# Kernel optimization log

Measured on AMD Instinct MI355X. Metric: run time of the kernel, lower is better.

Reference implementation:

```python
import jax, jax.numpy as jnp
import numpy as np

V, L_MAX, D_MODEL, N_LAYER, N_STATE, EXPAND = 49408, 512, 768, 4, 16, 2
D_INNER = EXPAND * D_MODEL            # 1536
DT_RANK = -(-D_MODEL // 16)           # 48 ('auto' = ceil(d_model/16))
D_CONV = 4
B, T = 4, 256
EPS = 1e-5


def setup_inputs() -> dict:
    key = jax.random.key(0)
    ks = jax.random.split(key, 10)
    s = 0.02
    inp = {
        "input_ids": jax.random.randint(ks[0], (B, T), 0, V),
        "emb": jax.random.normal(ks[1], (V, D_MODEL), jnp.float32) * s,
        "pos_emb": jax.random.normal(ks[2], (1, L_MAX, D_MODEL), jnp.float32) * s,
        "in_proj_w": jax.random.normal(ks[3], (N_LAYER, 2 * D_INNER, D_MODEL), jnp.float32) * s,
        "conv_w": jax.random.normal(ks[4], (N_LAYER, D_INNER, D_CONV), jnp.float32) * s,
        "conv_b": jnp.zeros((N_LAYER, D_INNER), jnp.float32),
        "x_proj_w": jax.random.normal(ks[5], (N_LAYER, DT_RANK + 2 * N_STATE, D_INNER), jnp.float32) * s,
        "dt_proj_w": jax.random.normal(ks[6], (N_LAYER, D_INNER, DT_RANK), jnp.float32) * s,
        "dt_proj_b": jnp.full((N_LAYER, D_INNER), -4.6, jnp.float32),  # softplus(-4.6)~0.01, inside [dt_min,dt_max]
        # S4D-real init: A_log[l,d,n] = log(n+1)
        "A_log": jnp.tile(jnp.log(jnp.arange(1, N_STATE + 1, dtype=jnp.float32)), (N_LAYER, D_INNER, 1)),
        "D_skip": jnp.ones((N_LAYER, D_INNER), jnp.float32),
        "out_proj_w": jax.random.normal(ks[7], (N_LAYER, D_MODEL, D_INNER), jnp.float32) * s,
        "norm_w": jnp.ones((D_MODEL,), jnp.float32),
    }
    return inp


def _causal_dwconv(x, w, b):
    # x: (B, C, T), w: (C, K) depthwise, b: (C,) ; causal pad K-1 on the left
    out = jax.lax.conv_general_dilated(
        x, w[:, None, :], window_strides=(1,), padding=[(D_CONV - 1, 0)],
        feature_group_count=x.shape[1], dimension_numbers=("NCH", "OIH", "NCH"))
    return out + b[None, :, None]


def _selective_scan(deltaA, dBx, Cm):
    # deltaA, dBx: (B, T, D, N); Cm: (B, T, N) -> y: (B, T, D)
    def step(h, t_in):
        dA, dbx, c = t_in
        h = dA * h + dbx                          # (B, D, N)
        y = jnp.einsum("bdn,bn->bd", h, c)
        return h, y
    h0 = jnp.zeros(deltaA.shape[:1] + deltaA.shape[2:], deltaA.dtype)
    _, ys = jax.lax.scan(step, h0, (deltaA.swapaxes(0, 1), dBx.swapaxes(0, 1), Cm.swapaxes(0, 1)))
    return ys.swapaxes(0, 1)


def _mamba_block(x, ipw, cw, cb, xpw, dpw, dpb, A_log, Dp, opw):
    # x: (B, T, d_model)
    xz = jnp.einsum("btd,ed->bte", x, ipw)        # (B, T, 2*D_INNER)
    xi, z = jnp.split(xz, 2, axis=-1)
    xi = jax.nn.silu(_causal_dwconv(xi.swapaxes(1, 2), cw, cb)).swapaxes(1, 2)  # (B, T, D_INNER)
    x_dbl = jnp.einsum("btd,ed->bte", xi, xpw)    # (B, T, DT_RANK + 2N)
    dt, Bm, Cm = jnp.split(x_dbl, [DT_RANK, DT_RANK + N_STATE], axis=-1)
    dt = jax.nn.softplus(jnp.einsum("btr,dr->btd", dt, dpw) + dpb)              # (B, T, D_INNER)
    A = -jnp.exp(A_log)                            # (D_INNER, N)
    deltaA = jnp.exp(dt[..., None] * A)            # (B, T, D_INNER, N)
    dBx = dt[..., None] * Bm[:, :, None, :] * xi[..., None]                     # (B, T, D_INNER, N)
    y = _selective_scan(deltaA, dBx, Cm) + Dp * xi
    y = y * jax.nn.silu(z)
    return jnp.einsum("btd,ed->bte", y, opw)       # (B, T, d_model)


def reference(input_ids, emb, pos_emb, in_proj_w, conv_w, conv_b, x_proj_w,
              dt_proj_w, dt_proj_b, A_log, D_skip, out_proj_w, norm_w):
    Tlen = input_ids.shape[1]
    x = emb[input_ids] + pos_emb[:, :Tlen, :]
    for l in range(N_LAYER):
        x = x + _mamba_block(x, in_proj_w[l], conv_w[l], conv_b[l], x_proj_w[l],
                             dt_proj_w[l], dt_proj_b[l], A_log[l], D_skip[l], out_proj_w[l])
    # RMSNormGated with no gate -> plain RMSNorm
    x = x * jax.lax.rsqrt(jnp.mean(x * x, axis=-1, keepdims=True) + EPS) * norm_w
    return x
```

## Files before the change

### kernel.cpp

```cpp
#include <hip/hip_runtime.h>
#include <math.h>

#define TLEN 256
#define BATCH 4
#define DMODEL 768
#define DINNER 1536
#define NSTATE 16
#define DTRANK 48
#define NLAYER 4
#define NTOK 1024

#define S_IP 2359296
#define S_OP 1179648
#define S_XP2 196608
#define WL (S_IP + S_OP + S_XP2)
#define NB_W (WL / 1024)
#define NB_WALL (NB_W * NLAYER)
#define NB_E (NTOK * DMODEL / 256)

typedef __bf16 bf16x8 __attribute__((ext_vector_type(8)));
typedef float f32x4 __attribute__((ext_vector_type(4)));

__device__ inline unsigned short f2b(float f) {
    union { float f; unsigned u; } v;
    v.f = f;
    unsigned r = (v.u + 0x7fffu + ((v.u >> 16) & 1u)) >> 16;
    return (unsigned short)r;
}
__device__ inline float b2f(unsigned short u) {
    union { unsigned u; float f; } v;
    v.u = ((unsigned)u) << 16;
    return v.f;
}

__device__ inline void gload16(const void* g, void* l) {
    __builtin_amdgcn_global_load_lds(
        (const __attribute__((address_space(1))) void*)g,
        (__attribute__((address_space(3))) void*)l, 16, 0, 0);
}

__device__ inline float red16(float p) {
    p += __int_as_float(__builtin_amdgcn_update_dpp(0, __float_as_int(p), 0xB1, 0xf, 0xf, true));
    p += __int_as_float(__builtin_amdgcn_update_dpp(0, __float_as_int(p), 0x4E, 0xf, 0xf, true));
    p += __int_as_float(__builtin_amdgcn_update_dpp(0, __float_as_int(p), 0x124, 0xf, 0xf, true));
    p += __int_as_float(__builtin_amdgcn_update_dpp(0, __float_as_int(p), 0x128, 0xf, 0xf, true));
    return p;
}

__global__ __launch_bounds__(256) void prep_k(const float* __restrict__ ipw,
                                              const float* __restrict__ opw,
                                              const float* __restrict__ xpw,
                                              const int* __restrict__ ids,
                                              const float* __restrict__ emb,
                                              const float* __restrict__ pos,
                                              unsigned short* __restrict__ w_all,
                                              float* __restrict__ x,
                                              unsigned short* __restrict__ xb) {
    int bid = blockIdx.x;
    int tid = threadIdx.x;
    if (bid >= NB_WALL) {
        int idx = (bid - NB_WALL) * 256 + tid;
        int d = idx % DMODEL;
        int bt = idx / DMODEL;
        int t = bt % TLEN;
        float v = emb[(size_t)ids[bt] * DMODEL + d] + pos[t * DMODEL + d];
        x[idx] = v;
        xb[idx] = f2b(v);
        return;
    }
    int l = bid / NB_W;
    int i4 = ((bid % NB_W) * 256 + tid) * 4;
    unsigned short* wl = w_all + (size_t)l * WL;
    if (i4 < S_IP) {
        float4 v = *(const float4*)(ipw + (size_t)l * S_IP + i4);
        ushort4 o; o.x = f2b(v.x); o.y = f2b(v.y); o.z = f2b(v.z); o.w = f2b(v.w);
        *(ushort4*)(wl + i4) = o;
    } else if (i4 < S_IP + S_OP) {
        int i = i4 - S_IP;
        float4 v = *(const float4*)(opw + (size_t)l * S_OP + i);
        ushort4 o; o.x = f2b(v.x); o.y = f2b(v.y); o.z = f2b(v.z); o.w = f2b(v.w);
        *(ushort4*)(wl + S_IP + i) = o;
    } else {
        int i = i4 - S_IP - S_OP;
        int r = i / 1536, k = i % 1536;
        ushort4 o = {0, 0, 0, 0};
        if (r < 80) {
            float4 v = *(const float4*)(xpw + (size_t)l * (80 * 1536) + (size_t)r * 1536 + k);
            o.x = f2b(v.x); o.y = f2b(v.y); o.z = f2b(v.z); o.w = f2b(v.w);
        }
        *(ushort4*)(wl + S_IP + S_OP + i) = o;
    }
}

__global__ __launch_bounds__(256) void ipgemm_k(const unsigned short* __restrict__ A,
                                                const unsigned short* __restrict__ B,
                                                unsigned short* __restrict__ o1) {
    __shared__ __align__(16) unsigned short Ab[2][128 * 64];
    __shared__ __align__(16) unsigned short Bb[2][128 * 64];

    int tid = threadIdx.x;
    int lane = tid & 63;
    int wave = tid >> 6;
    int wm = (wave >> 1) * 64;
    int wn = (wave & 1) * 64;
    int bm = blockIdx.x * 128;
    int bn = blockIdx.y * 128;
    int fr = lane & 15;
    int fq = lane >> 4;
    int fk = fq * 8;
    int srow = lane >> 3;
    int scol = (lane & 7) * 8;

    f32x4 acc[4][4] = {};

    auto stage = [&](int s, int k0) {
#pragma unroll
        for (int c = 0; c < 4; ++c) {
            int r = wave * 32 + c * 8;
            gload16(A + (size_t)(bm + r + srow) * DMODEL + k0 + scol, &Ab[s][r * 64]);
            gload16(B + (size_t)(bn + r + srow) * DMODEL + k0 + scol, &Bb[s][r * 64]);
        }
    };

    const int nk = DMODEL / 64;
    stage(0, 0);
    asm volatile("s_waitcnt vmcnt(0)" ::: "memory");
    __builtin_amdgcn_s_barrier();

    for (int t = 0; t < nk; ++t) {
        int cur = t & 1;
        if (t + 1 < nk) stage(cur ^ 1, (t + 1) * 64);
#pragma unroll
        for (int ks = 0; ks < 2; ++ks) {
            int kk = ks * 32 + fk;
            bf16x8 af[4], bfr[4];
#pragma unroll
            for (int i = 0; i < 4; ++i)
                af[i] = *(const bf16x8*)&Ab[cur][(wm + i * 16 + fr) * 64 + kk];
#pragma unroll
            for (int j = 0; j < 4; ++j)
                bfr[j] = *(const bf16x8*)&Bb[cur][(wn + j * 16 + fr) * 64 + kk];
#pragma unroll
            for (int i = 0; i < 4; ++i)
#pragma unroll
                for (int j = 0; j < 4; ++j)
                    acc[i][j] = __builtin_amdgcn_mfma_f32_16x16x32_bf16(
                        af[i], bfr[j], acc[i][j], 0, 0, 0);
        }
        asm volatile("s_waitcnt vmcnt(0)" ::: "memory");
        __builtin_amdgcn_s_barrier();
    }

#pragma unroll
    for (int i = 0; i < 4; ++i) {
#pragma unroll
        for (int j = 0; j < 4; ++j) {
            int lc = wn + j * 16 + fr;
#pragma unroll
            for (int q = 0; q < 4; ++q) {
                int lr = wm + i * 16 + fq * 4 + q;
                o1[(size_t)(bm + lr) * NTOK + bn + lc] = f2b(acc[i][j][q]);
            }
        }
    }
}

template <int MODE>
__global__ __launch_bounds__(256) void mgemm_k(const unsigned short* __restrict__ A, int lda,
                                               const unsigned short* __restrict__ B, int ldb,
                                               int K,
                                               float* __restrict__ o0,
                                               unsigned short* __restrict__ o1) {
    __shared__ __align__(16) unsigned short Ab[2][64 * 64];
    __shared__ __align__(16) unsigned short Bb[2][64 * 64];

    int tid = threadIdx.x;
    int lane = tid & 63;
    int wave = tid >> 6;
    int wm = (wave >> 1) * 32;
    int wn = (wave & 1) * 32;
    int bm = blockIdx.x * 64;
    int bn = blockIdx.y * 64;
    int fr = lane & 15;
    int fq = lane >> 4;
    int fk = fq * 8;
    int srow = lane >> 3;
    int scol = (lane & 7) * 8;

    f32x4 acc[2][2] = {};

    auto stage = [&](int s, int k0) {
#pragma unroll
        for (int c = 0; c < 2; ++c) {
            int r = wave * 16 + c * 8;
            gload16(A + (size_t)(bm + r + srow) * lda + k0 + scol, &Ab[s][r * 64]);
            gload16(B + (size_t)(bn + r + srow) * ldb + k0 + scol, &Bb[s][r * 64]);
        }
    };

    int nk = K >> 6;
    stage(0, 0);
    asm volatile("s_waitcnt vmcnt(0)" ::: "memory");
    __builtin_amdgcn_s_barrier();

    for (int t = 0; t < nk; ++t) {
        int cur = t & 1;
        if (t + 1 < nk) stage(cur ^ 1, (t + 1) * 64);
#pragma unroll
        for (int ks = 0; ks < 2; ++ks) {
            int kk = ks * 32 + fk;
            bf16x8 af[2], bfr[2];
#pragma unroll
            for (int i = 0; i < 2; ++i)
                af[i] = *(const bf16x8*)&Ab[cur][(wm + i * 16 + fr) * 64 + kk];
#pragma unroll
            for (int j = 0; j < 2; ++j)
                bfr[j] = *(const bf16x8*)&Bb[cur][(wn + j * 16 + fr) * 64 + kk];
#pragma unroll
            for (int i = 0; i < 2; ++i)
#pragma unroll
                for (int j = 0; j < 2; ++j)
                    acc[i][j] = __builtin_amdgcn_mfma_f32_16x16x32_bf16(
                        af[i], bfr[j], acc[i][j], 0, 0, 0);
        }
        asm volatile("s_waitcnt vmcnt(0)" ::: "memory");
        __builtin_amdgcn_s_barrier();
    }

#pragma unroll
    for (int i = 0; i < 2; ++i) {
#pragma unroll
        for (int j = 0; j < 2; ++j) {
            int lc = wn + j * 16 + fr;
#pragma unroll
            for (int q = 0; q < 4; ++q) {
                int lr = wm + i * 16 + fq * 4 + q;
                float v = acc[i][j][q];
                if (MODE == 1) {
                    int f = bm + lr;
                    if (f < 80) o0[(size_t)f * NTOK + bn + lc] = v;
                } else {
                    size_t idx = (size_t)(bm + lr) * DMODEL + bn + lc;
                    float nv = o0[idx] + v;
                    o0[idx] = nv;
                    o1[idx] = f2b(nv);
                }
            }
        }
    }
}

__global__ __launch_bounds__(256) void conv_k(const unsigned short* __restrict__ xzT,
                                              const float* __restrict__ cw,
                                              const float* __restrict__ cb,
                                              unsigned short* __restrict__ xib) {
    __shared__ unsigned short tile[4][256];
    int tid = threadIdx.x;
    int ch = tid >> 6;
    int d = blockIdx.x * 4 + ch;
    int b = blockIdx.y;
    int t0 = (tid & 63) * 4;
    const unsigned short* src = xzT + (size_t)d * NTOK + b * TLEN + t0;
    ushort4 cur = *(const ushort4*)src;
    ushort4 prev = {0, 0, 0, 0};
    if (t0 > 0) prev = *(const ushort4*)(src - 4);
    float w0 = cw[d * 4 + 0], w1 = cw[d * 4 + 1], w2 = cw[d * 4 + 2], w3 = cw[d * 4 + 3];
    float bb = cb[d];
    float xw[8] = {b2f(prev.x), b2f(prev.y), b2f(prev.z), b2f(prev.w),
                   b2f(cur.x), b2f(cur.y), b2f(cur.z), b2f(cur.w)};
#pragma unroll
    for (int u = 0; u < 4; ++u) {
        float s = bb + w0 * xw[u + 1] + w1 * xw[u + 2] + w2 * xw[u + 3] + w3 * xw[u + 4];
        float v = s / (1.f + __expf(-s));
        tile[ch][t0 + u] = f2b(v);
    }
    __syncthreads();
    int t = tid;
    ushort4 o;
    o.x = tile[0][t]; o.y = tile[1][t]; o.z = tile[2][t]; o.w = tile[3][t];
    *(ushort4*)(xib + (size_t)(b * TLEN + t) * DINNER + blockIdx.x * 4) = o;
}

__global__ __launch_bounds__(512) void scan_k(const unsigned short* __restrict__ xzT,
                                              const float* __restrict__ xdblT,
                                              const float* __restrict__ dpw,
                                              const float* __restrict__ dpb,
                                              const float* __restrict__ cw,
                                              const float* __restrict__ cb,
                                              const float* __restrict__ Alog,
                                              const float* __restrict__ Dsk,
                                              unsigned short* __restrict__ ybb) {
    __shared__ float dt_s[4][256];
    __shared__ float wdt_s[192];
    __shared__ float yl[4][260];
    __shared__ float cum[4][260];
    __shared__ float hL[8][4][16];
    __shared__ float Pb[8][4][16];
    __shared__ float Hin[8][4][16];

    int tid = threadIdx.x;
    int c = tid >> 6;
    int lane = tid & 63;
    int ch = lane >> 4;
    int n = lane & 15;
    int d0 = blockIdx.x * 4;
    int d = d0 + ch;
    int b = blockIdx.y;
    int tl0 = c * 32;

    if (tid < 192) wdt_s[tid] = dpw[(size_t)d0 * DTRANK + tid];
    __syncthreads();
    {
        int dd = tid >> 7;
        int tt = tid & 127;
        const float* wrow = &wdt_s[dd * DTRANK];
        const float* base = xdblT + (size_t)b * TLEN + tt;
        float a0 = 0.f, a1 = 0.f;
#pragma unroll 8
        for (int k = 0; k < DTRANK; ++k) {
            float w = wrow[k];
            a0 += w * base[(size_t)k * NTOK];
            a1 += w * base[(size_t)k * NTOK + 128];
        }
        float bias = dpb[d0 + dd];
        float v0 = a0 + bias, v1 = a1 + bias;
        v0 = (v0 > 0.f) ? v0 + log1pf(__expf(-v0)) : log1pf(__expf(v0));
        v1 = (v1 > 0.f) ? v1 + log1pf(__expf(-v1)) : log1pf(__expf(v1));
        dt_s[dd][tt] = v0;
        dt_s[dd][tt + 128] = v1;
    }
    __syncthreads();

    float a = -__expf(Alog[(size_t)d * NSTATE + n]);
    float Dv = Dsk[d];
    float w0 = cw[d * 4 + 0], w1 = cw[d * 4 + 1], w2 = cw[d * 4 + 2], w3 = cw[d * 4 + 3];
    float cbv = cb[d];
    const unsigned short* xzp = xzT + (size_t)d * NTOK + b * TLEN + tl0;
    const float* Bp = xdblT + (size_t)(DTRANK + n) * NTOK + b * TLEN + tl0;
    const float* Cp = xdblT + (size_t)(DTRANK + NSTATE + n) * NTOK + b * TLEN + tl0;

    float hm3 = 0.f, hm2 = 0.f, hm1 = 0.f;
    if (tl0 > 0) {
        ushort4 pv = *(const ushort4*)(xzp - 4);
        hm3 = b2f(pv.y); hm2 = b2f(pv.z); hm1 = b2f(pv.w);
    }

    float h = 0.f, cd = 0.f;
    for (int t8 = 0; t8 < 32; t8 += 8) {
        ushort4 xv0 = *(const ushort4*)(xzp + t8), xv1 = *(const ushort4*)(xzp + t8 + 4);
        float4 B0 = *(const float4*)(Bp + t8), B1 = *(const float4*)(Bp + t8 + 4);
        float4 C0 = *(const float4*)(Cp + t8), C1 = *(const float4*)(Cp + t8 + 4);
        float xw[11] = {hm3, hm2, hm1,
                        b2f(xv0.x), b2f(xv0.y), b2f(xv0.z), b2f(xv0.w),
                        b2f(xv1.x), b2f(xv1.y), b2f(xv1.z), b2f(xv1.w)};
        float Bs[8] = {B0.x, B0.y, B0.z, B0.w, B1.x, B1.y, B1.z, B1.w};
        float Cs[8] = {C0.x, C0.y, C0.z, C0.w, C1.x, C1.y, C1.z, C1.w};
#pragma unroll
        for (int u = 0; u < 8; ++u) {
            float sv = cbv + w0 * xw[u] + w1 * xw[u + 1] + w2 * xw[u + 2] + w3 * xw[u + 3];
            float xi = sv / (1.f + __expf(-sv));
            float dtv = dt_s[ch][tl0 + t8 + u];
            cd += dtv;
            float dA = __expf(dtv * a);
            h = dA * h + (dtv * xi) * Bs[u];
            float p = red16(h * Cs[u]);
            if (n == 0) {
                yl[ch][tl0 + t8 + u] = p + Dv * xi;
                cum[ch][tl0 + t8 + u] = cd;
            }
        }
        hm3 = xw[8]; hm2 = xw[9]; hm1 = xw[10];
    }
    hL[c][ch][n] = h;
    Pb[c][ch][n] = __expf(a * cd);
    __syncthreads();
    if (c == 0) {
        float H = 0.f;
        Hin[0][ch][n] = 0.f;
#pragma unroll
        for (int cc = 1; cc < 8; ++cc) {
            H = Pb[cc - 1][ch][n] * H + hL[cc - 1][ch][n];
            Hin[cc][ch][n] = H;
        }
    }
    __syncthreads();
    float Hv = Hin[c][ch][n];
    const unsigned short* zp = xzT + (size_t)(DINNER + d) * NTOK + b * TLEN + tl0;
    for (int t8 = 0; t8 < 32; t8 += 8) {
        float4 C0 = *(const float4*)(Cp + t8), C1 = *(const float4*)(Cp + t8 + 4);
        ushort4 zv0 = *(const ushort4*)(zp + t8), zv1 = *(const ushort4*)(zp + t8 + 4);
        float Cs[8] = {C0.x, C0.y, C0.z, C0.w, C1.x, C1.y, C1.z, C1.w};
        float zs[8] = {b2f(zv0.x), b2f(zv0.y), b2f(zv0.z), b2f(zv0.w),
                       b2f(zv1.x), b2f(zv1.y), b2f(zv1.z), b2f(zv1.w)};
#pragma unroll
        for (int u = 0; u < 8; ++u) {
            float cdt = cum[ch][tl0 + t8 + u];
            float corr = red16(Cs[u] * __expf(a * cdt) * Hv);
            if (n == 0) {
                float y = yl[ch][tl0 + t8 + u] + corr;
                float zz = zs[u];
                y *= zz / (1.f + __expf(-zz));
                yl[ch][tl0 + t8 + u] = y;
            }
        }
    }
    __syncthreads();
    if (tid < 256) {
        int t = tid;
        ushort4 o;
        o.x = f2b(yl[0][t]);
        o.y = f2b(yl[1][t]);
        o.z = f2b(yl[2][t]);
        o.w = f2b(yl[3][t]);
        *(ushort4*)(ybb + (size_t)(b * TLEN + t) * DINNER + blockIdx.x * 4) = o;
    }
}

__global__ __launch_bounds__(256) void rmsnorm_k(const float* __restrict__ x,
                                                 const float* __restrict__ nw,
                                                 float* __restrict__ out) {
    int row = blockIdx.x;
    const float* xr = x + (size_t)row * DMODEL;
    int tid = threadIdx.x;
    float s = 0.f;
    for (int d = tid; d < DMODEL; d += 256) {
        float v = xr[d];
        s += v * v;
    }
#pragma unroll
    for (int off = 32; off >= 1; off >>= 1) s += __shfl_down(s, off);
    __shared__ float red[4];
    __shared__ float scale;
    int wid = tid >> 6, lane = tid & 63;
    if (lane == 0) red[wid] = s;
    __syncthreads();
    if (tid == 0) {
        float tot = red[0] + red[1] + red[2] + red[3];
        scale = rsqrtf(tot / (float)DMODEL + 1e-5f);
    }
    __syncthreads();
    float sc = scale;
    for (int d = tid; d < DMODEL; d += 256)
        out[(size_t)row * DMODEL + d] = xr[d] * sc * nw[d];
}

extern "C" void kernel_launch(void* const* d_in, const int* in_sizes, int n_in,
                              void* d_out, int out_size, void* d_ws, size_t ws_size,
                              hipStream_t stream) {
    const int* ids = (const int*)d_in[0];
    const float* emb = (const float*)d_in[1];
    const float* pos = (const float*)d_in[2];
    const float* ipw = (const float*)d_in[3];
    const float* cw = (const float*)d_in[4];
    const float* cb = (const float*)d_in[5];
    const float* xpw = (const float*)d_in[6];
    const float* dpw = (const float*)d_in[7];
    const float* dpb = (const float*)d_in[8];
    const float* Alog = (const float*)d_in[9];
    const float* Dsk = (const float*)d_in[10];
    const float* opw = (const float*)d_in[11];
    const float* nw = (const float*)d_in[12];

    float* x = (float*)d_ws;
    float* xdblT = x + 786432;
    unsigned short* xb = (unsigned short*)(xdblT + 81920);
    unsigned short* xzT = xb + 786432;
    unsigned short* xib = xzT + 3145728;
    unsigned short* ybb = xib + 1572864;
    unsigned short* w_all = ybb + 1572864;

    prep_k<<<NB_WALL + NB_E, 256, 0, stream>>>(ipw, opw, xpw, ids, emb, pos,
                                               w_all, x, xb);

    for (int l = 0; l < NLAYER; ++l) {
        const unsigned short* w_ip = w_all + (size_t)l * WL;
        const unsigned short* w_op = w_ip + S_IP;
        const unsigned short* w_xp = w_op + S_OP;
        const float* cw_l = cw + (size_t)l * DINNER * 4;
        const float* cb_l = cb + (size_t)l * DINNER;
        const float* dpw_l = dpw + (size_t)l * DINNER * DTRANK;
        const float* dpb_l = dpb + (size_t)l * DINNER;
        const float* Alog_l = Alog + (size_t)l * DINNER * NSTATE;
        const float* Dsk_l = Dsk + (size_t)l * DINNER;

        ipgemm_k<<<dim3(3072 / 128, NTOK / 128), 256, 0, stream>>>(w_ip, xb, xzT);
        conv_k<<<dim3(DINNER / 4, BATCH), 256, 0, stream>>>(xzT, cw_l, cb_l, xib);
        mgemm_k<1><<<dim3(2, NTOK / 64), 256, 0, stream>>>(
            w_xp, DINNER, xib, DINNER, DINNER, xdblT, nullptr);
        scan_k<<<dim3(DINNER / 4, BATCH), 512, 0, stream>>>(
            xzT, xdblT, dpw_l, dpb_l, cw_l, cb_l, Alog_l, Dsk_l, ybb);
        mgemm_k<3><<<dim3(NTOK / 64, DMODEL / 64), 256, 0, stream>>>(
            ybb, DINNER, w_op, DINNER, DINNER, x, xb);
    }

    rmsnorm_k<<<NTOK, 256, 0, stream>>>(x, nw, (float*)d_out);
}
```

Before: 511.9 us.

## Triple-buffer GEMM LDS stages and XOR-swizzle LDS layout to avoid bank conflicts

New measurement: 501.9 us. No clear change (-2.0%).

```diff
diff --git a/kernel.cpp b/kernel.cpp
--- a/kernel.cpp
+++ b/kernel.cpp
@@ -95,8 +95,8 @@
 __global__ __launch_bounds__(256) void ipgemm_k(const unsigned short* __restrict__ A,
                                                 const unsigned short* __restrict__ B,
                                                 unsigned short* __restrict__ o1) {
-    __shared__ __align__(16) unsigned short Ab[2][128 * 64];
-    __shared__ __align__(16) unsigned short Bb[2][128 * 64];
+    __shared__ __align__(16) unsigned short Ab[3][128 * 64];
+    __shared__ __align__(16) unsigned short Bb[3][128 * 64];
 
     int tid = threadIdx.x;
     int lane = tid & 63;
@@ -110,6 +110,8 @@
     int fk = fq * 8;
     int srow = lane >> 3;
     int scol = (lane & 7) * 8;
+    int gcol = scol ^ (srow << 3);
+    int sw = (fr & 7) << 3;
 
     f32x4 acc[4][4] = {};
 
@@ -117,29 +119,34 @@
 #pragma unroll
         for (int c = 0; c < 4; ++c) {
             int r = wave * 32 + c * 8;
-            gload16(A + (size_t)(bm + r + srow) * DMODEL + k0 + scol, &Ab[s][r * 64]);
-            gload16(B + (size_t)(bn + r + srow) * DMODEL + k0 + scol, &Bb[s][r * 64]);
+            gload16(A + (size_t)(bm + r + srow) * DMODEL + k0 + gcol, &Ab[s][r * 64]);
+            gload16(B + (size_t)(bn + r + srow) * DMODEL + k0 + gcol, &Bb[s][r * 64]);
         }
     };
 
     const int nk = DMODEL / 64;
     stage(0, 0);
-    asm volatile("s_waitcnt vmcnt(0)" ::: "memory");
-    __builtin_amdgcn_s_barrier();
+    stage(1, 64);
 
     for (int t = 0; t < nk; ++t) {
-        int cur = t & 1;
-        if (t + 1 < nk) stage(cur ^ 1, (t + 1) * 64);
+        if (t + 1 < nk) {
+            asm volatile("s_waitcnt vmcnt(8)" ::: "memory");
+        } else {
+            asm volatile("s_waitcnt vmcnt(0)" ::: "memory");
+        }
+        __builtin_amdgcn_s_barrier();
+        if (t + 2 < nk) stage((t + 2) % 3, (t + 2) * 64);
+        int cur = t % 3;
 #pragma unroll
         for (int ks = 0; ks < 2; ++ks) {
             int kk = ks * 32 + fk;
             bf16x8 af[4], bfr[4];
 #pragma unroll
             for (int i = 0; i < 4; ++i)
-                af[i] = *(const bf16x8*)&Ab[cur][(wm + i * 16 + fr) * 64 + kk];
+                af[i] = *(const bf16x8*)&Ab[cur][(wm + i * 16 + fr) * 64 + (kk ^ sw)];
 #pragma unroll
             for (int j = 0; j < 4; ++j)
-                bfr[j] = *(const bf16x8*)&Bb[cur][(wn + j * 16 + fr) * 64 + kk];
+                bfr[j] = *(const bf16x8*)&Bb[cur][(wn + j * 16 + fr) * 64 + (kk ^ sw)];
 #pragma unroll
             for (int i = 0; i < 4; ++i)
 #pragma unroll
@@ -147,7 +154,6 @@
                     acc[i][j] = __builtin_amdgcn_mfma_f32_16x16x32_bf16(
                         af[i], bfr[j], acc[i][j], 0, 0, 0);
         }
-        asm volatile("s_waitcnt vmcnt(0)" ::: "memory");
         __builtin_amdgcn_s_barrier();
     }
 
@@ -171,8 +177,8 @@
                                                int K,
                                                float* __restrict__ o0,
                                                unsigned short* __restrict__ o1) {
-    __shared__ __align__(16) unsigned short Ab[2][64 * 64];
-    __shared__ __align__(16) unsigned short Bb[2][64 * 64];
+    __shared__ __align__(16) unsigned short Ab[3][64 * 64];
+    __shared__ __align__(16) unsigned short Bb[3][64 * 64];
 
     int tid = threadIdx.x;
     int lane = tid & 63;
@@ -186,6 +192,8 @@
     int fk = fq * 8;
     int srow = lane >> 3;
     int scol = (lane & 7) * 8;
+    int gcol = scol ^ (srow << 3);
+    int sw = (fr & 7) << 3;
 
     f32x4 acc[2][2] = {};
 
@@ -193,29 +201,34 @@
 #pragma unroll
         for (int c = 0; c < 2; ++c) {
             int r = wave * 16 + c * 8;
-            gload16(A + (size_t)(bm + r + srow) * lda + k0 + scol, &Ab[s][r * 64]);
-            gload16(B + (size_t)(bn + r + srow) * ldb + k0 + scol, &Bb[s][r * 64]);
+            gload16(A + (size_t)(bm + r + srow) * lda + k0 + gcol, &Ab[s][r * 64]);
+            gload16(B + (size_t)(bn + r + srow) * ldb + k0 + gcol, &Bb[s][r * 64]);
         }
     };
 
     int nk = K >> 6;
     stage(0, 0);
-    asm volatile("s_waitcnt vmcnt(0)" ::: "memory");
-    __builtin_amdgcn_s_barrier();
+    stage(1, 64);
 
     for (int t = 0; t < nk; ++t) {
-        int cur = t & 1;
-        if (t + 1 < nk) stage(cur ^ 1, (t + 1) * 64);
+        if (t + 1 < nk) {
+            asm volatile("s_waitcnt vmcnt(4)" ::: "memory");
+        } else {
+            asm volatile("s_waitcnt vmcnt(0)" ::: "memory");
+        }
+        __builtin_amdgcn_s_barrier();
+        if (t + 2 < nk) stage((t + 2) % 3, (t + 2) * 64);
+        int cur = t % 3;
 #pragma unroll
         for (int ks = 0; ks < 2; ++ks) {
             int kk = ks * 32 + fk;
             bf16x8 af[2], bfr[2];
 #pragma unroll
             for (int i = 0; i < 2; ++i)
-                af[i] = *(const bf16x8*)&Ab[cur][(wm + i * 16 + fr) * 64 + kk];
+                af[i] = *(const bf16x8*)&Ab[cur][(wm + i * 16 + fr) * 64 + (kk ^ sw)];
 #pragma unroll
             for (int j = 0; j < 2; ++j)
-                bfr[j] = *(const bf16x8*)&Bb[cur][(wn + j * 16 + fr) * 64 + kk];
+                bfr[j] = *(const bf16x8*)&Bb[cur][(wn + j * 16 + fr) * 64 + (kk ^ sw)];
 #pragma unroll
             for (int i = 0; i < 2; ++i)
 #pragma unroll
@@ -223,7 +236,6 @@
                     acc[i][j] = __builtin_amdgcn_mfma_f32_16x16x32_bf16(
                         af[i], bfr[j], acc[i][j], 0, 0, 0);
         }
-        asm volatile("s_waitcnt vmcnt(0)" ::: "memory");
         __builtin_amdgcn_s_barrier();
     }
 
```
